# Performance work log

Measured on AMD Instinct MI355X. Metric: run time of the kernel, lower is better.

Reference implementation:

```python
import jax, jax.numpy as jnp
import numpy as np

N = 100000       # nodes
E = 1600000      # edges
F_IN = 128       # input features
HID = 64         # hidden dim
CLS = 16         # classes


def setup_inputs() -> dict:
    key = jax.random.key(0)
    k = jax.random.split(key, 6)
    x = jax.random.normal(k[0], (N, F_IN), dtype=jnp.float32)
    src = jax.random.randint(k[1], (E,), 0, N, dtype=jnp.int32)
    dst = jax.random.randint(k[2], (E,), 0, N, dtype=jnp.int32)
    edge_index = jnp.stack([src, dst], axis=0)
    W1 = jax.random.normal(k[3], (F_IN, HID), dtype=jnp.float32) * (1.0 / np.sqrt(F_IN))
    b1 = jnp.zeros((HID,), dtype=jnp.float32)
    W2 = jax.random.normal(k[4], (HID, CLS), dtype=jnp.float32) * (1.0 / np.sqrt(HID))
    b2 = jnp.zeros((CLS,), dtype=jnp.float32)
    return {"x": x, "edge_index": edge_index, "W1": W1, "b1": b1, "W2": W2, "b2": b2}


def gcn_conv(x, W, b, src, dst, n_nodes):
    # GCNConv(normalize=True): h = W x; out_i = sum_{j->i} h_j / sqrt(d_i d_j) + h_i / d_i + b
    # (self-loops added with weight 1; deg includes the self-loop)
    h = x @ W                                             # [N, out]
    ones = jnp.ones(src.shape[0], dtype=x.dtype)
    deg = jax.ops.segment_sum(ones, dst, num_segments=n_nodes) + 1.0   # [N]
    dinv = deg ** -0.5
    norm = dinv[src] * dinv[dst]                          # [E]
    msg = h[src] * norm[:, None]                          # [E, out] gather
    out = jax.ops.segment_sum(msg, dst, num_segments=n_nodes)          # scatter-add
    out = out + h * (1.0 / deg)[:, None] + b              # self-loop term + bias
    return out


def reference(x, edge_index, W1, b1, W2, b2):
    src, dst = edge_index[0], edge_index[1]
    n = x.shape[0]
    h = jax.nn.relu(gcn_conv(x, W1, b1, src, dst, n))
    # dropout(p=0.5) is identity in eval mode
    h = jax.nn.relu(gcn_conv(h, W2, b2, src, dst, n))
    return jax.nn.log_softmax(h, axis=-1)
```

## Files before the change

kernel.cpp:

```cpp
#include <hip/hip_runtime.h>
#include <hip/hip_bf16.h>


typedef unsigned short u16;
typedef __attribute__((ext_vector_type(8))) short short8;
typedef __attribute__((ext_vector_type(4))) float f32x4;

#define CAP 4096

__device__ __forceinline__ float bf2f(u16 u) {
  return __uint_as_float(((unsigned int)u) << 16);
}
__device__ __forceinline__ u16 f2bf(float f) {
  unsigned int u = __float_as_uint(f);
  u += 0x7fffu + ((u >> 16) & 1u);
  return (u16)(u >> 16);
}

__global__ __launch_bounds__(512) void kpartc(
    const int* __restrict__ src, const int* __restrict__ dst,
    int* __restrict__ cursor, int* __restrict__ etmp,
    const void* __restrict__ W1r, const void* __restrict__ b1r,
    const void* __restrict__ W2r, const void* __restrict__ b2r,
    u16* __restrict__ W1b, float* __restrict__ b1f, u16* __restrict__ W2b,
    float* __restrict__ b2f, int* __restrict__ mode, int E, int NB) {
  __shared__ int hist[1024], basep[1024];
  __shared__ float red[8];
  __shared__ int smode;
  int tid = threadIdx.x;

  if (blockIdx.x == 0) {
    const u16* w = (const u16*)W1r;
    float mx = 0.f;
    for (int i = tid; i < 8192; i += 512) {
      float av = fabsf(bf2f(w[i]));
      if (!(av <= 1e6f)) av = 3e38f;
      mx = fmaxf(mx, av);
    }
    #pragma unroll
    for (int off = 32; off >= 1; off >>= 1) mx = fmaxf(mx, __shfl_xor(mx, off, 64));
    if ((tid & 63) == 0) red[tid >> 6] = mx;
    __syncthreads();
    if (tid == 0) {
      float m2 = 0.f;
      #pragma unroll
      for (int wv = 0; wv < 8; ++wv) m2 = fmaxf(m2, red[wv]);
      smode = (m2 > 1e6f) ? 1 : 0;
      mode[0] = smode;
    }
    __syncthreads();
    int m = smode;
    for (int i = tid; i < 8192; i += 512)
      W1b[i] = m ? f2bf(((const float*)W1r)[i]) : ((const u16*)W1r)[i];
    for (int i = tid; i < 1024; i += 512)
      W2b[i] = m ? f2bf(((const float*)W2r)[i]) : ((const u16*)W2r)[i];
    if (tid < 64) b1f[tid] = m ? ((const float*)b1r)[tid] : bf2f(((const u16*)b1r)[tid]);
    if (tid < 16) b2f[tid] = m ? ((const float*)b2r)[tid] : bf2f(((const u16*)b2r)[tid]);
    return;
  }

  for (int i = tid; i < 1024; i += 512) hist[i] = 0;
  __syncthreads();
  int e0 = (blockIdx.x - 1) * 8192 + tid * 16;
  int pk[16], off[16], cb[16];
  if (e0 + 15 < E) {
    int4 s4[4], d4[4];
    #pragma unroll
    for (int u = 0; u < 4; ++u) {
      s4[u] = ((const int4*)(src + e0))[u];
      d4[u] = ((const int4*)(dst + e0))[u];
    }
    const int* sp = (const int*)s4;
    const int* dp = (const int*)d4;
    #pragma unroll
    for (int k = 0; k < 16; ++k) {
      int s = sp[k], d = dp[k];
      cb[k] = d >> 7;
      pk[k] = (s << 7) | (d & 127);
      off[k] = atomicAdd(&hist[cb[k]], 1);
    }
  } else {
    #pragma unroll
    for (int k = 0; k < 16; ++k) {
      int e = e0 + k;
      cb[k] = -1;
      if (e < E) {
        int s = src[e], d = dst[e];
        cb[k] = d >> 7;
        pk[k] = (s << 7) | (d & 127);
        off[k] = atomicAdd(&hist[cb[k]], 1);
      }
    }
  }
  __syncthreads();
  for (int i = tid; i < NB; i += 512)
    if (hist[i]) basep[i] = atomicAdd(&cursor[i], hist[i]);
  __syncthreads();
  if (e0 + 15 < E) {
    #pragma unroll
    for (int k = 0; k < 16; ++k)
      etmp[cb[k] * CAP + basep[cb[k]] + off[k]] = pk[k];
  } else {
    #pragma unroll
    for (int k = 0; k < 16; ++k)
      if (cb[k] >= 0) etmp[cb[k] * CAP + basep[cb[k]] + off[k]] = pk[k];
  }
}

__global__ __launch_bounds__(512) void kfine(const int* __restrict__ etmp,
                                             const int* __restrict__ cursor,
                                             float* __restrict__ dinv, int N) {
  __shared__ int hist[128];
  int bk = blockIdx.x, tid = threadIdx.x;
  int cnt = cursor[bk], base = bk * CAP;
  if (tid < 128) hist[tid] = 0;
  __syncthreads();
  for (int i = tid; i < cnt; i += 512)
    atomicAdd(&hist[etmp[base + i] & 127], 1);
  __syncthreads();
  int node = (bk << 7) + tid;
  if (tid < 128 && node < N)
    dinv[node] = rsqrtf((float)(hist[tid] + 1));
}

__global__ __launch_bounds__(256) void kgemm1(const void* __restrict__ xraw,
                                              const u16* __restrict__ W1b,
                                              const int* __restrict__ mode,
                                              const float* __restrict__ dinv,
                                              u16* __restrict__ h1s, int n) {
  int mflag = mode[0];
  int wid = blockIdx.x * 4 + (threadIdx.x >> 6);
  int row0 = wid * 16;
  if (row0 >= n) return;
  int lane = threadIdx.x & 63;
  int m = lane & 15, q = lane >> 4;

  short8 bfrag[4][4];
  for (int jb = 0; jb < 4; ++jb)
    for (int kb = 0; kb < 4; ++kb) {
      short8 f;
      #pragma unroll
      for (int j = 0; j < 8; ++j)
        f[j] = (short)W1b[(kb * 32 + q * 8 + j) * 64 + jb * 16 + m];
      bfrag[jb][kb] = f;
    }

  f32x4 acc[4];
  #pragma unroll
  for (int jb = 0; jb < 4; ++jb) acc[jb] = (f32x4){0.f, 0.f, 0.f, 0.f};

  #pragma unroll
  for (int kb = 0; kb < 4; ++kb) {
    short8 a;
    if (mflag) {
      const float* xf = (const float*)xraw + (size_t)(row0 + m) * 128 + kb * 32 + q * 8;
      float4 u0 = ((const float4*)xf)[0];
      float4 u1 = ((const float4*)xf)[1];
      __hip_bfloat162 p0 = __float22bfloat162_rn(make_float2(u0.x, u0.y));
      __hip_bfloat162 p1 = __float22bfloat162_rn(make_float2(u0.z, u0.w));
      __hip_bfloat162 p2 = __float22bfloat162_rn(make_float2(u1.x, u1.y));
      __hip_bfloat162 p3 = __float22bfloat162_rn(make_float2(u1.z, u1.w));
      unsigned int w0 = *(const unsigned int*)&p0;
      unsigned int w1 = *(const unsigned int*)&p1;
      unsigned int w2 = *(const unsigned int*)&p2;
      unsigned int w3 = *(const unsigned int*)&p3;
      a[0] = (short)(w0 & 0xffff); a[1] = (short)(w0 >> 16);
      a[2] = (short)(w1 & 0xffff); a[3] = (short)(w1 >> 16);
      a[4] = (short)(w2 & 0xffff); a[5] = (short)(w2 >> 16);
      a[6] = (short)(w3 & 0xffff); a[7] = (short)(w3 >> 16);
    } else {
      a = *(const short8*)((const u16*)xraw + (size_t)(row0 + m) * 128 + kb * 32 + q * 8);
    }
    #pragma unroll
    for (int jb = 0; jb < 4; ++jb)
      acc[jb] = __builtin_amdgcn_mfma_f32_16x16x32_bf16(a, bfrag[jb][kb], acc[jb], 0, 0, 0);
  }

  #pragma unroll
  for (int r = 0; r < 4; ++r) {
    float dv = dinv[row0 + q * 4 + r];
    #pragma unroll
    for (int jb = 0; jb < 4; ++jb)
      h1s[(row0 + q * 4 + r) * 64 + jb * 16 + m] = f2bf(acc[jb][r] * dv);
  }
}

__global__ __launch_bounds__(512) void kagg1f(
    const u16* __restrict__ h1s, const int* __restrict__ etmp,
    const int* __restrict__ cursor, const float* __restrict__ dinv,
    const float* __restrict__ b1f, const u16* __restrict__ W2b,
    int* __restrict__ esort, int2* __restrict__ rowse,
    u16* __restrict__ h2sb, int N) {
  __shared__ int eL[CAP];
  __shared__ int eS[CAP];
  __shared__ int hist[128], starts[128], curs[128];
  __shared__ float sdinv[128];

  int tid = threadIdx.x;
  int bk = blockIdx.x;
  int base = bk * CAP;
  int cnt = cursor[bk];
  int node0 = bk << 7;

  if (tid < 128) {
    hist[tid] = 0;
    int nd = node0 + tid;
    sdinv[tid] = (nd < N) ? dinv[nd] : 0.f;
  }
  __syncthreads();
  for (int i = tid; i < cnt; i += 512) {
    int pk = etmp[base + i];
    eL[i] = pk;
    atomicAdd(&hist[pk & 127], 1);
  }
  __syncthreads();
  if (tid < 64) {
    int v0 = hist[tid], v1 = hist[tid + 64];
    int s0 = v0;
    #pragma unroll
    for (int off = 1; off < 64; off <<= 1) {
      int t = __shfl_up(s0, off, 64);
      if (tid >= off) s0 += t;
    }
    int tot0 = __shfl(s0, 63, 64);
    int s1 = v1;
    #pragma unroll
    for (int off = 1; off < 64; off <<= 1) {
      int t = __shfl_up(s1, off, 64);
      if (tid >= off) s1 += t;
    }
    s1 += tot0;
    int e0x = s0 - v0, e1x = s1 - v1;
    starts[tid] = e0x;  curs[tid] = e0x;
    starts[tid + 64] = e1x;  curs[tid + 64] = e1x;
    int n0 = node0 + tid, n1 = n0 + 64;
    if (n0 < N) rowse[n0] = make_int2(base + e0x, base + e0x + v0);
    if (n1 < N) rowse[n1] = make_int2(base + e1x, base + e1x + v1);
  }
  __syncthreads();
  for (int i = tid; i < cnt; i += 512) {
    int pk = eL[i];
    int pos = atomicAdd(&curs[pk & 127], 1);
    int sidx = pk >> 7;
    eS[pos] = sidx;
    esort[base + pos] = sidx;
  }

  int lane = tid & 63, wv = tid >> 6;
  int m16 = lane & 15, q = lane >> 4;
  short8 bw0, bw1;
  #pragma unroll
  for (int j = 0; j < 8; ++j) {
    bw0[j] = (short)W2b[(q * 8 + j) * 16 + m16];
    bw1[j] = (short)W2b[(32 + q * 8 + j) * 16 + m16];
  }
  __syncthreads();

  float* rowsL = (float*)eL;
  const uint4* h1u = (const uint4*)h1s;
  int fl = m16 & 7, hl = m16 >> 3;
  int wrow = wv * 4 + q;

  for (int pass = 0; pass < 4; ++pass) {
    int nl = pass * 32 + wv * 4 + q;
    int nd = node0 + nl;
    int cn = (nd < N) ? nd : node0;
    int rs = starts[nl], ke = rs + hist[nl];
    float a0 = 0.f, a1 = 0.f, a2 = 0.f, a3 = 0.f;
    float a4 = 0.f, a5 = 0.f, a6 = 0.f, a7 = 0.f;
    int k = rs;
    for (; k + 8 <= ke; k += 8) {
      int i0 = eS[k + hl], i1 = eS[k + 2 + hl];
      int i2 = eS[k + 4 + hl], i3 = eS[k + 6 + hl];
      uint4 g0 = h1u[i0 * 8 + fl];
      uint4 g1 = h1u[i1 * 8 + fl];
      uint4 g2 = h1u[i2 * 8 + fl];
      uint4 g3 = h1u[i3 * 8 + fl];
      a0 += bf2f((u16)(g0.x & 0xffff)) + bf2f((u16)(g1.x & 0xffff))
          + bf2f((u16)(g2.x & 0xffff)) + bf2f((u16)(g3.x & 0xffff));
      a1 += bf2f((u16)(g0.x >> 16)) + bf2f((u16)(g1.x >> 16))
          + bf2f((u16)(g2.x >> 16)) + bf2f((u16)(g3.x >> 16));
      a2 += bf2f((u16)(g0.y & 0xffff)) + bf2f((u16)(g1.y & 0xffff))
          + bf2f((u16)(g2.y & 0xffff)) + bf2f((u16)(g3.y & 0xffff));
      a3 += bf2f((u16)(g0.y >> 16)) + bf2f((u16)(g1.y >> 16))
          + bf2f((u16)(g2.y >> 16)) + bf2f((u16)(g3.y >> 16));
      a4 += bf2f((u16)(g0.z & 0xffff)) + bf2f((u16)(g1.z & 0xffff))
          + bf2f((u16)(g2.z & 0xffff)) + bf2f((u16)(g3.z & 0xffff));
      a5 += bf2f((u16)(g0.z >> 16)) + bf2f((u16)(g1.z >> 16))
          + bf2f((u16)(g2.z >> 16)) + bf2f((u16)(g3.z >> 16));
      a6 += bf2f((u16)(g0.w & 0xffff)) + bf2f((u16)(g1.w & 0xffff))
          + bf2f((u16)(g2.w & 0xffff)) + bf2f((u16)(g3.w & 0xffff));
      a7 += bf2f((u16)(g0.w >> 16)) + bf2f((u16)(g1.w >> 16))
          + bf2f((u16)(g2.w >> 16)) + bf2f((u16)(g3.w >> 16));
    }
    for (; k < ke; k += 2) {
      int e = k + hl;
      bool valid = e < ke;
      uint4 g = h1u[eS[valid ? e : (ke - 1)] * 8 + fl];
      if (valid) {
        a0 += bf2f((u16)(g.x & 0xffff));  a1 += bf2f((u16)(g.x >> 16));
        a2 += bf2f((u16)(g.y & 0xffff));  a3 += bf2f((u16)(g.y >> 16));
        a4 += bf2f((u16)(g.z & 0xffff));  a5 += bf2f((u16)(g.z >> 16));
        a6 += bf2f((u16)(g.w & 0xffff));  a7 += bf2f((u16)(g.w >> 16));
      }
    }
    a0 += __shfl_xor(a0, 8, 16);  a1 += __shfl_xor(a1, 8, 16);
    a2 += __shfl_xor(a2, 8, 16);  a3 += __shfl_xor(a3, 8, 16);
    a4 += __shfl_xor(a4, 8, 16);  a5 += __shfl_xor(a5, 8, 16);
    a6 += __shfl_xor(a6, 8, 16);  a7 += __shfl_xor(a7, 8, 16);

    uint4 sg = h1u[cn * 8 + fl];
    float dv = sdinv[nl];
    float4 ba = ((const float4*)b1f)[2 * fl];
    float4 bb = ((const float4*)b1f)[2 * fl + 1];
    float v0 = fmaxf(dv * (a0 + bf2f((u16)(sg.x & 0xffff))) + ba.x, 0.f);
    float v1 = fmaxf(dv * (a1 + bf2f((u16)(sg.x >> 16))) + ba.y, 0.f);
    float v2 = fmaxf(dv * (a2 + bf2f((u16)(sg.y & 0xffff))) + ba.z, 0.f);
    float v3 = fmaxf(dv * (a3 + bf2f((u16)(sg.y >> 16))) + ba.w, 0.f);
    float v4 = fmaxf(dv * (a4 + bf2f((u16)(sg.z & 0xffff))) + bb.x, 0.f);
    float v5 = fmaxf(dv * (a5 + bf2f((u16)(sg.z >> 16))) + bb.y, 0.f);
    float v6 = fmaxf(dv * (a6 + bf2f((u16)(sg.w & 0xffff))) + bb.z, 0.f);
    float v7 = fmaxf(dv * (a7 + bf2f((u16)(sg.w >> 16))) + bb.w, 0.f);

    if (hl == 0) {
      float* rp = &rowsL[wrow * 68 + 8 * fl];
      *(float4*)rp = make_float4(v0, v1, v2, v3);
      *(float4*)(rp + 4) = make_float4(v4, v5, v6, v7);
    }
    __builtin_amdgcn_wave_barrier();

    const float* ar = &rowsL[(wv * 4 + (m16 & 3)) * 68];
    bool rv = (m16 < 4);
    short8 af0, af1;
    #pragma unroll
    for (int j = 0; j < 8; ++j) {
      af0[j] = rv ? (short)f2bf(ar[q * 8 + j]) : (short)0;
      af1[j] = rv ? (short)f2bf(ar[32 + q * 8 + j]) : (short)0;
    }
    f32x4 c = (f32x4){0.f, 0.f, 0.f, 0.f};
    c = __builtin_amdgcn_mfma_f32_16x16x32_bf16(af0, bw0, c, 0, 0, 0);
    c = __builtin_amdgcn_mfma_f32_16x16x32_bf16(af1, bw1, c, 0, 0, 0);
    if (q == 0) {
      #pragma unroll
      for (int r = 0; r < 4; ++r) {
        int nl2 = pass * 32 + wv * 4 + r;
        int nd2 = node0 + nl2;
        if (nd2 < N) h2sb[nd2 * 16 + m16] = f2bf(c[r] * sdinv[nl2]);
      }
    }
    __builtin_amdgcn_wave_barrier();
  }
}

__global__ __launch_bounds__(256) void kagg2(
    const u16* __restrict__ h2sb, const int* __restrict__ esort,
    const int2* __restrict__ rowse, const float* __restrict__ dinv,
    const float* __restrict__ b2f, const int* __restrict__ mode,
    void* __restrict__ out, int n) {
  int mflag = mode[0];
  int tid = threadIdx.x;
  int lane = tid & 63, wv = tid >> 6;
  int oc = lane >> 3, ol = lane & 7;
  int hl = ol >> 2, fl = ol & 3;
  int node = blockIdx.x * 32 + wv * 8 + oc;
  if (node >= n) node = n - 1;
  int2 se = rowse[node];
  int beg = se.x, end = se.y;
  const uint2* h2v = (const uint2*)h2sb;
  uint2 sg = h2v[node * 4 + fl];
  float a0 = 0.f, a1 = 0.f, a2 = 0.f, a3 = 0.f;

  int k = beg;
  for (; k + 8 <= end; k += 8) {
    int i0 = esort[k + hl], i1 = esort[k + 2 + hl];
    int i2 = esort[k + 4 + hl], i3 = esort[k + 6 + hl];
    uint2 g0 = h2v[i0 * 4 + fl];
    uint2 g1 = h2v[i1 * 4 + fl];
    uint2 g2 = h2v[i2 * 4 + fl];
    uint2 g3 = h2v[i3 * 4 + fl];
    a0 += bf2f((u16)(g0.x & 0xffff)) + bf2f((u16)(g1.x & 0xffff))
        + bf2f((u16)(g2.x & 0xffff)) + bf2f((u16)(g3.x & 0xffff));
    a1 += bf2f((u16)(g0.x >> 16)) + bf2f((u16)(g1.x >> 16))
        + bf2f((u16)(g2.x >> 16)) + bf2f((u16)(g3.x >> 16));
    a2 += bf2f((u16)(g0.y & 0xffff)) + bf2f((u16)(g1.y & 0xffff))
        + bf2f((u16)(g2.y & 0xffff)) + bf2f((u16)(g3.y & 0xffff));
    a3 += bf2f((u16)(g0.y >> 16)) + bf2f((u16)(g1.y >> 16))
        + bf2f((u16)(g2.y >> 16)) + bf2f((u16)(g3.y >> 16));
  }
  for (; k < end; k += 2) {
    int e = k + hl;
    bool valid = e < end;
    uint2 g = h2v[esort[valid ? e : (end - 1)] * 4 + fl];
    if (valid) {
      a0 += bf2f((u16)(g.x & 0xffff));  a1 += bf2f((u16)(g.x >> 16));
      a2 += bf2f((u16)(g.y & 0xffff));  a3 += bf2f((u16)(g.y >> 16));
    }
  }
  a0 += __shfl_xor(a0, 4, 8);  a1 += __shfl_xor(a1, 4, 8);
  a2 += __shfl_xor(a2, 4, 8);  a3 += __shfl_xor(a3, 4, 8);

  float dv = dinv[node];
  float4 bv = ((const float4*)b2f)[fl];
  float v0 = fmaxf(dv * (a0 + bf2f((u16)(sg.x & 0xffff))) + bv.x, 0.f);
  float v1 = fmaxf(dv * (a1 + bf2f((u16)(sg.x >> 16))) + bv.y, 0.f);
  float v2 = fmaxf(dv * (a2 + bf2f((u16)(sg.y & 0xffff))) + bv.z, 0.f);
  float v3 = fmaxf(dv * (a3 + bf2f((u16)(sg.y >> 16))) + bv.w, 0.f);

  float m = fmaxf(fmaxf(v0, v1), fmaxf(v2, v3));
  m = fmaxf(m, __shfl_xor(m, 1, 4));
  m = fmaxf(m, __shfl_xor(m, 2, 4));
  float ex = __expf(v0 - m) + __expf(v1 - m) + __expf(v2 - m) + __expf(v3 - m);
  ex += __shfl_xor(ex, 1, 4);
  ex += __shfl_xor(ex, 2, 4);
  float lg = __logf(ex);
  float r0 = v0 - m - lg, r1 = v1 - m - lg;
  float r2 = v2 - m - lg, r3 = v3 - m - lg;
  if (hl == 0) {
    if (mflag) {
      ((float4*)out)[(size_t)node * 4 + fl] = make_float4(r0, r1, r2, r3);
    } else {
      uint2 o;
      o.x = (unsigned int)f2bf(r0) | ((unsigned int)f2bf(r1) << 16);
      o.y = (unsigned int)f2bf(r2) | ((unsigned int)f2bf(r3) << 16);
      ((uint2*)out)[(size_t)node * 4 + fl] = o;
    }
  }
}

extern "C" void kernel_launch(void* const* d_in, const int* in_sizes, int n_in,
                              void* d_out, int out_size, void* d_ws, size_t ws_size,
                              hipStream_t stream) {
  const void* x  = d_in[0];
  const int* ei  = (const int*)d_in[1];
  const void* W1 = d_in[2];
  const void* b1 = d_in[3];
  const void* W2 = d_in[4];
  const void* b2 = d_in[5];

  const int N = in_sizes[0] / 128;
  const int E = in_sizes[1] / 2;
  const int* src = ei;
  const int* dst = ei + E;
  const int NB = (N + 127) >> 7;

  char* ws = (char*)d_ws;
  size_t off = 0;
  auto alloc = [&](size_t bytes) -> char* {
    char* p = ws + off;
    off = (off + bytes + 255) & ~(size_t)255;
    return p;
  };
  u16*   h1s    = (u16*)  alloc((size_t)N * 64 * 2);
  u16*   h2sb   = (u16*)  alloc((size_t)N * 16 * 2);
  int*   etmp   = (int*)  alloc((size_t)NB * CAP * 4);
  int*   esort  = (int*)  alloc((size_t)NB * CAP * 4);
  int2*  rowse  = (int2*) alloc((size_t)N * 8);
  float* dinv   = (float*)alloc((size_t)N * 4);
  int*   cursor = (int*)  alloc((size_t)NB * 4);
  u16*   W1b    = (u16*)  alloc(8192 * 2);
  u16*   W2b    = (u16*)  alloc(1024 * 2);
  float* b1f    = (float*)alloc(64 * 4);
  float* b2f    = (float*)alloc(16 * 4);
  int*   mode   = (int*)  alloc(4);

  hipMemsetAsync(cursor, 0, (size_t)NB * 4, stream);

  int pblocks = (E + 8191) / 8192;
  kpartc<<<pblocks + 1, 512, 0, stream>>>(src, dst, cursor, etmp,
                                          W1, b1, W2, b2,
                                          W1b, b1f, W2b, b2f, mode, E, NB);
  kfine<<<NB, 512, 0, stream>>>(etmp, cursor, dinv, N);

  int tiles = (N + 15) / 16;
  kgemm1<<<(tiles + 3) / 4, 256, 0, stream>>>(x, W1b, mode, dinv, h1s, N);
  kagg1f<<<NB, 512, 0, stream>>>(h1s, etmp, cursor, dinv, b1f, W2b,
                                 esort, rowse, h2sb, N);
  kagg2<<<(N + 31) / 32, 256, 0, stream>>>(h2sb, esort, rowse, dinv, b2f, mode,
                                           d_out, N);
}
```

Measured before the change: 197.6 us.

## Fuse degree count into GEMM1 and restructure layer-1 gather per lane

Merges the per-bucket degree histogram kernel into the first GEMM kernel, so each 128-node bucket computes its dinv in shared memory and then runs 8 waves of 16-row MFMA tiles. This removes one launch and a global round-trip of dinv. Row indices are clamped and stores are guarded for the tail. In the layer-1 aggregation, each of 16 lanes now loads 4 features (uint2) per edge with 8 edges in flight, replacing the two-half split with 8 features per lane and the cross-lane shuffle reduction. The trade-off is narrower loads and more per-edge index reads.

```diff
diff --git a/kernel.cpp b/kernel.cpp
--- a/kernel.cpp
+++ b/kernel.cpp
@@ -107,33 +107,36 @@
   }
 }
 
-__global__ __launch_bounds__(512) void kfine(const int* __restrict__ etmp,
-                                             const int* __restrict__ cursor,
-                                             float* __restrict__ dinv, int N) {
+__global__ __launch_bounds__(512) void kgemm1f(
+    const void* __restrict__ xraw, const u16* __restrict__ W1b,
+    const int* __restrict__ mode, const int* __restrict__ etmp,
+    const int* __restrict__ cursor, float* __restrict__ dinv,
+    u16* __restrict__ h1s, int N) {
   __shared__ int hist[128];
-  int bk = blockIdx.x, tid = threadIdx.x;
-  int cnt = cursor[bk], base = bk * CAP;
+  __shared__ float sdinv[128];
+  int tid = threadIdx.x;
+  int bk = blockIdx.x;
+  int base = bk * CAP;
+  int cnt = cursor[bk];
+  int node0 = bk << 7;
+
   if (tid < 128) hist[tid] = 0;
   __syncthreads();
   for (int i = tid; i < cnt; i += 512)
     atomicAdd(&hist[etmp[base + i] & 127], 1);
   __syncthreads();
-  int node = (bk << 7) + tid;
-  if (tid < 128 && node < N)
-    dinv[node] = rsqrtf((float)(hist[tid] + 1));
-}
-
-__global__ __launch_bounds__(256) void kgemm1(const void* __restrict__ xraw,
-                                              const u16* __restrict__ W1b,
-                                              const int* __restrict__ mode,
-                                              const float* __restrict__ dinv,
-                                              u16* __restrict__ h1s, int n) {
+  if (tid < 128) {
+    float dv = rsqrtf((float)(hist[tid] + 1));
+    sdinv[tid] = dv;
+    int nd = node0 + tid;
+    if (nd < N) dinv[nd] = dv;
+  }
+  __syncthreads();
+
   int mflag = mode[0];
-  int wid = blockIdx.x * 4 + (threadIdx.x >> 6);
-  int row0 = wid * 16;
-  if (row0 >= n) return;
-  int lane = threadIdx.x & 63;
+  int lane = tid & 63, wv = tid >> 6;
   int m = lane & 15, q = lane >> 4;
+  int row0 = node0 + wv * 16;
 
   short8 bfrag[4][4];
   for (int jb = 0; jb < 4; ++jb)
@@ -149,11 +152,13 @@
   #pragma unroll
   for (int jb = 0; jb < 4; ++jb) acc[jb] = (f32x4){0.f, 0.f, 0.f, 0.f};
 
+  int rowm = row0 + m;
+  size_t rc = (size_t)((rowm < N) ? rowm : (N - 1));
   #pragma unroll
   for (int kb = 0; kb < 4; ++kb) {
     short8 a;
     if (mflag) {
-      const float* xf = (const float*)xraw + (size_t)(row0 + m) * 128 + kb * 32 + q * 8;
+      const float* xf = (const float*)xraw + rc * 128 + kb * 32 + q * 8;
       float4 u0 = ((const float4*)xf)[0];
       float4 u1 = ((const float4*)xf)[1];
       __hip_bfloat162 p0 = __float22bfloat162_rn(make_float2(u0.x, u0.y));
@@ -169,7 +174,7 @@
       a[4] = (short)(w2 & 0xffff); a[5] = (short)(w2 >> 16);
       a[6] = (short)(w3 & 0xffff); a[7] = (short)(w3 >> 16);
     } else {
-      a = *(const short8*)((const u16*)xraw + (size_t)(row0 + m) * 128 + kb * 32 + q * 8);
+      a = *(const short8*)((const u16*)xraw + rc * 128 + kb * 32 + q * 8);
     }
     #pragma unroll
     for (int jb = 0; jb < 4; ++jb)
@@ -178,10 +183,13 @@
 
   #pragma unroll
   for (int r = 0; r < 4; ++r) {
-    float dv = dinv[row0 + q * 4 + r];
-    #pragma unroll
-    for (int jb = 0; jb < 4; ++jb)
-      h1s[(row0 + q * 4 + r) * 64 + jb * 16 + m] = f2bf(acc[jb][r] * dv);
+    int rr = row0 + q * 4 + r;
+    if (rr < N) {
+      float dv = sdinv[wv * 16 + q * 4 + r];
+      #pragma unroll
+      for (int jb = 0; jb < 4; ++jb)
+        h1s[(size_t)rr * 64 + jb * 16 + m] = f2bf(acc[jb][r] * dv);
+    }
   }
 }
 
@@ -257,8 +265,8 @@
   __syncthreads();
 
   float* rowsL = (float*)eL;
-  const uint4* h1u = (const uint4*)h1s;
-  int fl = m16 & 7, hl = m16 >> 3;
+  const uint2* h1v = (const uint2*)h1s;
+  int ql = m16;
   int wrow = wv * 4 + q;
 
   for (int pass = 0; pass < 4; ++pass) {
@@ -267,66 +275,40 @@
     int cn = (nd < N) ? nd : node0;
     int rs = starts[nl], ke = rs + hist[nl];
     float a0 = 0.f, a1 = 0.f, a2 = 0.f, a3 = 0.f;
-    float a4 = 0.f, a5 = 0.f, a6 = 0.f, a7 = 0.f;
     int k = rs;
     for (; k + 8 <= ke; k += 8) {
-      int i0 = eS[k + hl], i1 = eS[k + 2 + hl];
-      int i2 = eS[k + 4 + hl], i3 = eS[k + 6 + hl];
-      uint4 g0 = h1u[i0 * 8 + fl];
-      uint4 g1 = h1u[i1 * 8 + fl];
-      uint4 g2 = h1u[i2 * 8 + fl];
-      uint4 g3 = h1u[i3 * 8 + fl];
-      a0 += bf2f((u16)(g0.x & 0xffff)) + bf2f((u16)(g1.x & 0xffff))
-          + bf2f((u16)(g2.x & 0xffff)) + bf2f((u16)(g3.x & 0xffff));
-      a1 += bf2f((u16)(g0.x >> 16)) + bf2f((u16)(g1.x >> 16))
-          + bf2f((u16)(g2.x >> 16)) + bf2f((u16)(g3.x >> 16));
-      a2 += bf2f((u16)(g0.y & 0xffff)) + bf2f((u16)(g1.y & 0xffff))
-          + bf2f((u16)(g2.y & 0xffff)) + bf2f((u16)(g3.y & 0xffff));
-      a3 += bf2f((u16)(g0.y >> 16)) + bf2f((u16)(g1.y >> 16))
-          + bf2f((u16)(g2.y >> 16)) + bf2f((u16)(g3.y >> 16));
-      a4 += bf2f((u16)(g0.z & 0xffff)) + bf2f((u16)(g1.z & 0xffff))
-          + bf2f((u16)(g2.z & 0xffff)) + bf2f((u16)(g3.z & 0xffff));
-      a5 += bf2f((u16)(g0.z >> 16)) + bf2f((u16)(g1.z >> 16))
-          + bf2f((u16)(g2.z >> 16)) + bf2f((u16)(g3.z >> 16));
-      a6 += bf2f((u16)(g0.w & 0xffff)) + bf2f((u16)(g1.w & 0xffff))
-          + bf2f((u16)(g2.w & 0xffff)) + bf2f((u16)(g3.w & 0xffff));
-      a7 += bf2f((u16)(g0.w >> 16)) + bf2f((u16)(g1.w >> 16))
-          + bf2f((u16)(g2.w >> 16)) + bf2f((u16)(g3.w >> 16));
-    }
-    for (; k < ke; k += 2) {
-      int e = k + hl;
-      bool valid = e < ke;
-      uint4 g = h1u[eS[valid ? e : (ke - 1)] * 8 + fl];
-      if (valid) {
-        a0 += bf2f((u16)(g.x & 0xffff));  a1 += bf2f((u16)(g.x >> 16));
-        a2 += bf2f((u16)(g.y & 0xffff));  a3 += bf2f((u16)(g.y >> 16));
-        a4 += bf2f((u16)(g.z & 0xffff));  a5 += bf2f((u16)(g.z >> 16));
-        a6 += bf2f((u16)(g.w & 0xffff));  a7 += bf2f((u16)(g.w >> 16));
+      int sI[8];
+      uint2 g[8];
+      #pragma unroll
+      for (int p = 0; p < 8; ++p) sI[p] = eS[k + p];
+      #pragma unroll
+      for (int p = 0; p < 8; ++p) g[p] = h1v[sI[p] * 16 + ql];
+      #pragma unroll
+      for (int p = 0; p < 8; ++p) {
+        a0 += bf2f((u16)(g[p].x & 0xffff));
+        a1 += bf2f((u16)(g[p].x >> 16));
+        a2 += bf2f((u16)(g[p].y & 0xffff));
+        a3 += bf2f((u16)(g[p].y >> 16));
       }
     }
-    a0 += __shfl_xor(a0, 8, 16);  a1 += __shfl_xor(a1, 8, 16);
-    a2 += __shfl_xor(a2, 8, 16);  a3 += __shfl_xor(a3, 8, 16);
-    a4 += __shfl_xor(a4, 8, 16);  a5 += __shfl_xor(a5, 8, 16);
-    a6 += __shfl_xor(a6, 8, 16);  a7 += __shfl_xor(a7, 8, 16);
-
-    uint4 sg = h1u[cn * 8 + fl];
+    for (; k < ke; ++k) {
+      int s = eS[k];
+      uint2 g = h1v[s * 16 + ql];
+      a0 += bf2f((u16)(g.x & 0xffff));
+      a1 += bf2f((u16)(g.x >> 16));
+      a2 += bf2f((u16)(g.y & 0xffff));
+      a3 += bf2f((u16)(g.y >> 16));
+    }
+    uint2 sg = h1v[cn * 16 + ql];
     float dv = sdinv[nl];
-    float4 ba = ((const float4*)b1f)[2 * fl];
-    float4 bb = ((const float4*)b1f)[2 * fl + 1];
-    float v0 = fmaxf(dv * (a0 + bf2f((u16)(sg.x & 0xffff))) + ba.x, 0.f);
-    float v1 = fmaxf(dv * (a1 + bf2f((u16)(sg.x >> 16))) + ba.y, 0.f);
-    float v2 = fmaxf(dv * (a2 + bf2f((u16)(sg.y & 0xffff))) + ba.z, 0.f);
-    float v3 = fmaxf(dv * (a3 + bf2f((u16)(sg.y >> 16))) + ba.w, 0.f);
-    float v4 = fmaxf(dv * (a4 + bf2f((u16)(sg.z & 0xffff))) + bb.x, 0.f);
-    float v5 = fmaxf(dv * (a5 + bf2f((u16)(sg.z >> 16))) + bb.y, 0.f);
-    float v6 = fmaxf(dv * (a6 + bf2f((u16)(sg.w & 0xffff))) + bb.z, 0.f);
-    float v7 = fmaxf(dv * (a7 + bf2f((u16)(sg.w >> 16))) + bb.w, 0.f);
-
-    if (hl == 0) {
-      float* rp = &rowsL[wrow * 68 + 8 * fl];
-      *(float4*)rp = make_float4(v0, v1, v2, v3);
-      *(float4*)(rp + 4) = make_float4(v4, v5, v6, v7);
-    }
+    float4 bv = ((const float4*)b1f)[ql];
+    float4 vr;
+    vr.x = fmaxf(dv * (a0 + bf2f((u16)(sg.x & 0xffff))) + bv.x, 0.f);
+    vr.y = fmaxf(dv * (a1 + bf2f((u16)(sg.x >> 16))) + bv.y, 0.f);
+    vr.z = fmaxf(dv * (a2 + bf2f((u16)(sg.y & 0xffff))) + bv.z, 0.f);
+    vr.w = fmaxf(dv * (a3 + bf2f((u16)(sg.y >> 16))) + bv.w, 0.f);
+
+    *(float4*)&rowsL[wrow * 68 + 4 * ql] = vr;
     __builtin_amdgcn_wave_barrier();
 
     const float* ar = &rowsL[(wv * 4 + (m16 & 3)) * 68];
@@ -469,10 +451,7 @@
   kpartc<<<pblocks + 1, 512, 0, stream>>>(src, dst, cursor, etmp,
                                           W1, b1, W2, b2,
                                           W1b, b1f, W2b, b2f, mode, E, NB);
-  kfine<<<NB, 512, 0, stream>>>(etmp, cursor, dinv, N);
-
-  int tiles = (N + 15) / 16;
-  kgemm1<<<(tiles + 3) / 4, 256, 0, stream>>>(x, W1b, mode, dinv, h1s, N);
+  kgemm1f<<<NB, 512, 0, stream>>>(x, W1b, mode, etmp, cursor, dinv, h1s, N);
   kagg1f<<<NB, 512, 0, stream>>>(h1s, etmp, cursor, dinv, b1f, W2b,
                                  esort, rowse, h2sb, N);
   kagg2<<<(N + 31) / 32, 256, 0, stream>>>(h2sb, esort, rowse, dinv, b2f, mode,
```

New measurement: 196.7 us. Within noise of the previous version (-0.4%).
